# Kernel optimization log

Measured on AMD Instinct MI355X. Metric: run time of the kernel, lower is better.

The kernel has to match this reference:

```python
import jax, jax.numpy as jnp
import numpy as np

B, T, D, H = 8192, 1024, 16, 16

def setup_inputs() -> dict:
    key = jax.random.key(0)
    k1, k2, k3, k4 = jax.random.split(key, 4)
    x = jax.random.normal(k1, (B, T, D), dtype=jnp.float32)
    # fused LSTM params: gate order (i, f, g, o)
    Wi = jax.random.normal(k2, (D, 4 * H), dtype=jnp.float32) * (1.0 / np.sqrt(D))
    Wh = jax.random.normal(k3, (H, 4 * H), dtype=jnp.float32) * (1.0 / np.sqrt(H))
    b = jnp.zeros((4 * H,), dtype=jnp.float32)
    Wd = jax.random.normal(k4, (H, 2), dtype=jnp.float32) * (1.0 / np.sqrt(H))
    bd = jnp.zeros((2,), dtype=jnp.float32)
    return {"x": x, "Wi": Wi, "Wh": Wh, "b": b, "Wd": Wd, "bd": bd}

def reference(x, Wi, Wh, b, Wd, bd):
    Bx = x.shape[0]
    Hh = Wh.shape[0]
    c0 = jnp.zeros((Bx, Hh), dtype=x.dtype)
    h0 = jnp.zeros((Bx, Hh), dtype=x.dtype)

    def step(carry, x_t):
        c, h = carry
        z = x_t @ Wi + h @ Wh + b  # [B, 4H]
        i, f, g, o = jnp.split(z, 4, axis=-1)
        c = jax.nn.sigmoid(f) * c + jax.nn.sigmoid(i) * jnp.tanh(g)
        h = jax.nn.sigmoid(o) * jnp.tanh(c)
        return (c, h), None

    (c_T, h_T), _ = jax.lax.scan(step, (c0, h0), jnp.swapaxes(x, 0, 1))
    # NOTE: the original flax model uses carry1[0], the CELL state c, for the head
    logits = c_T @ Wd + bd
    return jax.nn.softmax(logits, axis=-1)
```

## Files before the change

### kernel.cpp

```cpp
#include <hip/hip_runtime.h>
#include <math.h>
#include <stdint.h>


#define BB 8192
#define TT 1024
#define DD 16
#define HH 16

typedef __attribute__((ext_vector_type(8))) short short8;
typedef __attribute__((ext_vector_type(4))) float f32x4;

__device__ __forceinline__ short f2bf(float f) {
    uint32_t u = __builtin_bit_cast(uint32_t, f);
    u += 0x7fffu + ((u >> 16) & 1u);
    return (short)(u >> 16);
}

__global__ __launch_bounds__(64) void carry_lstm_mfma(
    const float* __restrict__ x,
    const float* __restrict__ Wi,
    const float* __restrict__ Wh,
    const float* __restrict__ b,
    const float* __restrict__ Wd,
    const float* __restrict__ bd,
    float* __restrict__ out)
{
    __shared__ __align__(16) char smem[1536];
    const int lane = threadIdx.x;
    const int n = lane & 15;
    const int q = lane >> 4;
    const int e0 = blockIdx.x * 16;

    short8 Bg[4];
    float bias[4];
#pragma unroll
    for (int g = 0; g < 4; ++g) {
#pragma unroll
        for (int j = 0; j < 8; ++j) {
            const int row = q * 8 + j;
            const float w = (row < 16) ? Wi[row * 64 + g * 16 + n]
                                       : Wh[(row - 16) * 64 + g * 16 + n];
            Bg[g][j] = f2bf(w);
        }
        bias[g] = b[g * 16 + n];
    }

    const float* xg = x + (size_t)(e0 + n) * (TT * DD) + q * 4;
    char* xw = &smem[n * 48 + q * 8];
    const short8* afp = (const short8*)&smem[(q >> 1) * 768 + n * 48 + (q & 1) * 16];

    *(uint2*)&smem[768 + n * 48 + q * 8] = make_uint2(0u, 0u);
    {
        float4 x0 = *(const float4*)(xg);
        uint32_t lo = (uint16_t)f2bf(x0.x) | ((uint32_t)(uint16_t)f2bf(x0.y) << 16);
        uint32_t hi = (uint16_t)f2bf(x0.z) | ((uint32_t)(uint16_t)f2bf(x0.w) << 16);
        *(uint2*)xw = make_uint2(lo, hi);
    }
    float4 xf = *(const float4*)(xg + DD);

    float cr[4] = {0.f, 0.f, 0.f, 0.f};

    for (int t = 0; t < TT; ++t) {
        short8 af = *afp;
        asm volatile("" ::: "memory");

        f32x4 acc0 = {bias[0], bias[0], bias[0], bias[0]};
        f32x4 acc1 = {bias[1], bias[1], bias[1], bias[1]};
        f32x4 acc2 = {bias[2], bias[2], bias[2], bias[2]};
        f32x4 acc3 = {bias[3], bias[3], bias[3], bias[3]};
        acc0 = __builtin_amdgcn_mfma_f32_16x16x32_bf16(af, Bg[0], acc0, 0, 0, 0);
        acc1 = __builtin_amdgcn_mfma_f32_16x16x32_bf16(af, Bg[1], acc1, 0, 0, 0);
        acc2 = __builtin_amdgcn_mfma_f32_16x16x32_bf16(af, Bg[2], acc2, 0, 0, 0);
        acc3 = __builtin_amdgcn_mfma_f32_16x16x32_bf16(af, Bg[3], acc3, 0, 0, 0);

        const int t2 = (t + 2 < TT) ? (t + 2) : (TT - 1);
        const float4 xf2 = *(const float4*)(xg + (size_t)t2 * DD);

#pragma unroll
        for (int r = 0; r < 4; ++r) {
            float zi = acc0[r], zf = acc1[r], zg = acc2[r], zo = acc3[r];
            zi = fmaxf(zi, -12.f); zf = fmaxf(zf, -12.f);
            zg = fmaxf(zg, -12.f); zo = fmaxf(zo, -12.f);
            const float ea = __expf(-zi);
            const float ef = __expf(-zf);
            const float G  = __expf(-2.f * zg);
            const float eo = __expf(-zo);
            float u = fmaf(cr[r], ea, cr[r]);
            u = fmaf(u, G, u);
            const float s  = 1.f - G;
            const float s2 = fmaf(s, ef, s);
            const float num = u + s2;
            const float den = ((ea + 1.f) * (ef + 1.f));
            const float den3 = fmaf(den, G, den);
            const float cn = num * __builtin_amdgcn_rcpf(den3);
            cr[r] = cn;
            const float cc = fmaxf(cn, -12.f);
            const float C2 = __expf(-2.f * cc);
            const float hd = (1.f + C2) * (1.f + eo);
            const float h  = (1.f - C2) * __builtin_amdgcn_rcpf(hd);
            *(short*)&smem[768 + (q * 4 + r) * 48 + n * 2] = f2bf(h);
        }

        {
            uint32_t lo = (uint16_t)f2bf(xf.x) | ((uint32_t)(uint16_t)f2bf(xf.y) << 16);
            uint32_t hi = (uint16_t)f2bf(xf.z) | ((uint32_t)(uint16_t)f2bf(xf.w) << 16);
            *(uint2*)xw = make_uint2(lo, hi);
        }
        xf = xf2;
        asm volatile("" ::: "memory");
    }

    float p0[4], p1[4];
    const float wd0 = Wd[n * 2 + 0], wd1 = Wd[n * 2 + 1];
#pragma unroll
    for (int r = 0; r < 4; ++r) { p0[r] = cr[r] * wd0; p1[r] = cr[r] * wd1; }
#pragma unroll
    for (int off = 1; off < 16; off <<= 1) {
#pragma unroll
        for (int r = 0; r < 4; ++r) {
            p0[r] += __shfl_xor(p0[r], off, 16);
            p1[r] += __shfl_xor(p1[r], off, 16);
        }
    }
#pragma unroll
    for (int r = 0; r < 4; ++r) {
        if (n == r) {
            const float l0 = p0[r] + bd[0];
            const float l1 = p1[r] + bd[1];
            const float m  = fmaxf(l0, l1);
            const float E0 = __expf(l0 - m), E1 = __expf(l1 - m);
            const float inv = __builtin_amdgcn_rcpf(E0 + E1);
            const size_t e = (size_t)(e0 + q * 4 + r);
            out[e * 2 + 0] = E0 * inv;
            out[e * 2 + 1] = E1 * inv;
        }
    }
}

extern "C" void kernel_launch(void* const* d_in, const int* in_sizes, int n_in,
                              void* d_out, int out_size, void* d_ws, size_t ws_size,
                              hipStream_t stream) {
    const float* x  = (const float*)d_in[0];
    const float* Wi = (const float*)d_in[1];
    const float* Wh = (const float*)d_in[2];
    const float* b  = (const float*)d_in[3];
    const float* Wd = (const float*)d_in[4];
    const float* bd = (const float*)d_in[5];
    float* out = (float*)d_out;

    hipLaunchKernelGGL(carry_lstm_mfma, dim3(BB / 16), dim3(64), 0, stream,
                       x, Wi, Wh, b, Wd, bd, out);
}
```

Before: 1.181 ms.

## Keep LSTM hidden state in registers via transposed fp16 MFMA, split input projection

Transposes the gate GEMM so the MFMA output layout matches the next step's B operand, letting h stay in registers and removing the per-step shared-memory round trip. The input projection x@Wi+b is computed one step ahead with separate 16x16x16 fp16 MFMAs off the recurrent critical path. The -log2(e) scaling is folded into the weights so raw v_exp_f32 can be used, and x is prefetched through an 8-deep register ring. It switches the operands from bf16 to fp16 with round-toward-zero conversion, which changes rounding behaviour.

```diff
diff --git a/kernel.cpp b/kernel.cpp
--- a/kernel.cpp
+++ b/kernel.cpp
@@ -8,13 +8,16 @@
 #define DD 16
 #define HH 16
 
-typedef __attribute__((ext_vector_type(8))) short short8;
+typedef __attribute__((ext_vector_type(4))) __fp16 half4;
+typedef __attribute__((ext_vector_type(2))) __fp16 half2;
 typedef __attribute__((ext_vector_type(4))) float f32x4;
 
-__device__ __forceinline__ short f2bf(float f) {
-    uint32_t u = __builtin_bit_cast(uint32_t, f);
-    u += 0x7fffu + ((u >> 16) & 1u);
-    return (short)(u >> 16);
+#define L2E 1.4426950408889634f
+#define CL1 17.312340490667555f
+#define CL2 34.624680981335110f
+
+__device__ __forceinline__ float ex2(float xx) {
+    float r; asm("v_exp_f32 %0, %1" : "=v"(r) : "v"(xx)); return r;
 }
 
 __global__ __launch_bounds__(64) void carry_lstm_mfma(
@@ -26,115 +29,107 @@
     const float* __restrict__ bd,
     float* __restrict__ out)
 {
-    __shared__ __align__(16) char smem[1536];
     const int lane = threadIdx.x;
-    const int n = lane & 15;
-    const int q = lane >> 4;
-    const int e0 = blockIdx.x * 16;
+    const int lo4  = lane & 15;
+    const int s4   = lane >> 4;
+    const int e0   = blockIdx.x * 16;
 
-    short8 Bg[4];
-    float bias[4];
+    half4 Ax[4], Ah[4];
+    f32x4 bias[4];
 #pragma unroll
     for (int g = 0; g < 4; ++g) {
+        const float sc = (g == 2) ? (-2.f * L2E) : (-L2E);
+#pragma unroll
+        for (int e = 0; e < 4; ++e) {
+            const int k = 4 * s4 + e;
+            Ax[g][e] = (__fp16)(Wi[k * 64 + g * 16 + lo4] * sc);
+            Ah[g][e] = (__fp16)(Wh[k * 64 + g * 16 + lo4] * sc);
+        }
+#pragma unroll
+        for (int r = 0; r < 4; ++r)
+            bias[g][r] = b[g * 16 + 4 * s4 + r] * sc;
+    }
+
+    const float* xp = x + (size_t)(e0 + lo4) * (TT * DD) + s4 * 4;
+    float4 xq[8];
+#pragma unroll
+    for (int j = 0; j < 8; ++j) xq[j] = *(const float4*)(xp + j * 16);
+
+    union H4 { half4 v; half2 h[2]; };
+    H4 b0;
+    b0.h[0] = __builtin_amdgcn_cvt_pkrtz(xq[0].x, xq[0].y);
+    b0.h[1] = __builtin_amdgcn_cvt_pkrtz(xq[0].z, xq[0].w);
+    f32x4 ax0 = __builtin_amdgcn_mfma_f32_16x16x16f16(Ax[0], b0.v, bias[0], 0, 0, 0);
+    f32x4 ax1 = __builtin_amdgcn_mfma_f32_16x16x16f16(Ax[1], b0.v, bias[1], 0, 0, 0);
+    f32x4 ax2 = __builtin_amdgcn_mfma_f32_16x16x16f16(Ax[2], b0.v, bias[2], 0, 0, 0);
+    f32x4 ax3 = __builtin_amdgcn_mfma_f32_16x16x16f16(Ax[3], b0.v, bias[3], 0, 0, 0);
+
+    half4 Bh = {};
+    float cr[4] = {0.f, 0.f, 0.f, 0.f};
+    const float* xpp = xp + 8 * 16;
+
+    for (int tb = 0; tb < TT; tb += 8) {
+        const float* lp = (tb + 16 <= TT) ? xpp : xp;
 #pragma unroll
         for (int j = 0; j < 8; ++j) {
-            const int row = q * 8 + j;
-            const float w = (row < 16) ? Wi[row * 64 + g * 16 + n]
-                                       : Wh[(row - 16) * 64 + g * 16 + n];
-            Bg[g][j] = f2bf(w);
+            f32x4 aI = __builtin_amdgcn_mfma_f32_16x16x16f16(Ah[0], Bh, ax0, 0, 0, 0);
+            f32x4 aF = __builtin_amdgcn_mfma_f32_16x16x16f16(Ah[1], Bh, ax1, 0, 0, 0);
+            f32x4 aG = __builtin_amdgcn_mfma_f32_16x16x16f16(Ah[2], Bh, ax2, 0, 0, 0);
+            f32x4 aO = __builtin_amdgcn_mfma_f32_16x16x16f16(Ah[3], Bh, ax3, 0, 0, 0);
+
+            xq[j] = *(const float4*)(lp + j * 16);
+            const float4 xn = xq[(j + 1) & 7];
+            H4 bx;
+            bx.h[0] = __builtin_amdgcn_cvt_pkrtz(xn.x, xn.y);
+            bx.h[1] = __builtin_amdgcn_cvt_pkrtz(xn.z, xn.w);
+            ax0 = __builtin_amdgcn_mfma_f32_16x16x16f16(Ax[0], bx.v, bias[0], 0, 0, 0);
+            ax1 = __builtin_amdgcn_mfma_f32_16x16x16f16(Ax[1], bx.v, bias[1], 0, 0, 0);
+            ax2 = __builtin_amdgcn_mfma_f32_16x16x16f16(Ax[2], bx.v, bias[2], 0, 0, 0);
+            ax3 = __builtin_amdgcn_mfma_f32_16x16x16f16(Ax[3], bx.v, bias[3], 0, 0, 0);
+
+            float hh[4];
+#pragma unroll
+            for (int r = 0; r < 4; ++r) {
+                const float ea = ex2(fminf(aI[r], CL1));
+                const float ef = ex2(fminf(aF[r], CL1));
+                const float G  = ex2(fminf(aG[r], CL2));
+                const float eo = ex2(fminf(aO[r], CL1));
+                float u = fmaf(cr[r], ea, cr[r]);
+                u = fmaf(u, G, u);
+                const float s  = 1.f - G;
+                const float s2 = fmaf(s, ef, s);
+                const float num = u + s2;
+                const float den = (ea + 1.f) * (ef + 1.f);
+                const float den3 = fmaf(den, G, den);
+                const float cn = num * __builtin_amdgcn_rcpf(den3);
+                cr[r] = cn;
+                const float C2 = ex2(fminf(cn * (-2.f * L2E), CL2));
+                const float hd = (1.f + C2) * (1.f + eo);
+                hh[r] = (1.f - C2) * __builtin_amdgcn_rcpf(hd);
+            }
+            H4 hu;
+            hu.h[0] = __builtin_amdgcn_cvt_pkrtz(hh[0], hh[1]);
+            hu.h[1] = __builtin_amdgcn_cvt_pkrtz(hh[2], hh[3]);
+            Bh = hu.v;
         }
-        bias[g] = b[g * 16 + n];
+        xpp += 8 * 16;
     }
 
-    const float* xg = x + (size_t)(e0 + n) * (TT * DD) + q * 4;
-    char* xw = &smem[n * 48 + q * 8];
-    const short8* afp = (const short8*)&smem[(q >> 1) * 768 + n * 48 + (q & 1) * 16];
-
-    *(uint2*)&smem[768 + n * 48 + q * 8] = make_uint2(0u, 0u);
-    {
-        float4 x0 = *(const float4*)(xg);
-        uint32_t lo = (uint16_t)f2bf(x0.x) | ((uint32_t)(uint16_t)f2bf(x0.y) << 16);
-        uint32_t hi = (uint16_t)f2bf(x0.z) | ((uint32_t)(uint16_t)f2bf(x0.w) << 16);
-        *(uint2*)xw = make_uint2(lo, hi);
-    }
-    float4 xf = *(const float4*)(xg + DD);
-
-    float cr[4] = {0.f, 0.f, 0.f, 0.f};
-
-    for (int t = 0; t < TT; ++t) {
-        short8 af = *afp;
-        asm volatile("" ::: "memory");
-
-        f32x4 acc0 = {bias[0], bias[0], bias[0], bias[0]};
-        f32x4 acc1 = {bias[1], bias[1], bias[1], bias[1]};
-        f32x4 acc2 = {bias[2], bias[2], bias[2], bias[2]};
-        f32x4 acc3 = {bias[3], bias[3], bias[3], bias[3]};
-        acc0 = __builtin_amdgcn_mfma_f32_16x16x32_bf16(af, Bg[0], acc0, 0, 0, 0);
-        acc1 = __builtin_amdgcn_mfma_f32_16x16x32_bf16(af, Bg[1], acc1, 0, 0, 0);
-        acc2 = __builtin_amdgcn_mfma_f32_16x16x32_bf16(af, Bg[2], acc2, 0, 0, 0);
-        acc3 = __builtin_amdgcn_mfma_f32_16x16x32_bf16(af, Bg[3], acc3, 0, 0, 0);
-
-        const int t2 = (t + 2 < TT) ? (t + 2) : (TT - 1);
-        const float4 xf2 = *(const float4*)(xg + (size_t)t2 * DD);
-
-#pragma unroll
-        for (int r = 0; r < 4; ++r) {
-            float zi = acc0[r], zf = acc1[r], zg = acc2[r], zo = acc3[r];
-            zi = fmaxf(zi, -12.f); zf = fmaxf(zf, -12.f);
-            zg = fmaxf(zg, -12.f); zo = fmaxf(zo, -12.f);
-            const float ea = __expf(-zi);
-            const float ef = __expf(-zf);
-            const float G  = __expf(-2.f * zg);
-            const float eo = __expf(-zo);
-            float u = fmaf(cr[r], ea, cr[r]);
-            u = fmaf(u, G, u);
-            const float s  = 1.f - G;
-            const float s2 = fmaf(s, ef, s);
-            const float num = u + s2;
-            const float den = ((ea + 1.f) * (ef + 1.f));
-            const float den3 = fmaf(den, G, den);
-            const float cn = num * __builtin_amdgcn_rcpf(den3);
-            cr[r] = cn;
-            const float cc = fmaxf(cn, -12.f);
-            const float C2 = __expf(-2.f * cc);
-            const float hd = (1.f + C2) * (1.f + eo);
-            const float h  = (1.f - C2) * __builtin_amdgcn_rcpf(hd);
-            *(short*)&smem[768 + (q * 4 + r) * 48 + n * 2] = f2bf(h);
-        }
-
-        {
-            uint32_t lo = (uint16_t)f2bf(xf.x) | ((uint32_t)(uint16_t)f2bf(xf.y) << 16);
-            uint32_t hi = (uint16_t)f2bf(xf.z) | ((uint32_t)(uint16_t)f2bf(xf.w) << 16);
-            *(uint2*)xw = make_uint2(lo, hi);
-        }
-        xf = xf2;
-        asm volatile("" ::: "memory");
-    }
-
-    float p0[4], p1[4];
-    const float wd0 = Wd[n * 2 + 0], wd1 = Wd[n * 2 + 1];
-#pragma unroll
-    for (int r = 0; r < 4; ++r) { p0[r] = cr[r] * wd0; p1[r] = cr[r] * wd1; }
-#pragma unroll
-    for (int off = 1; off < 16; off <<= 1) {
-#pragma unroll
-        for (int r = 0; r < 4; ++r) {
-            p0[r] += __shfl_xor(p0[r], off, 16);
-            p1[r] += __shfl_xor(p1[r], off, 16);
-        }
-    }
+    float p0 = 0.f, p1 = 0.f;
 #pragma unroll
     for (int r = 0; r < 4; ++r) {
-        if (n == r) {
-            const float l0 = p0[r] + bd[0];
-            const float l1 = p1[r] + bd[1];
-            const float m  = fmaxf(l0, l1);
-            const float E0 = __expf(l0 - m), E1 = __expf(l1 - m);
-            const float inv = __builtin_amdgcn_rcpf(E0 + E1);
-            const size_t e = (size_t)(e0 + q * 4 + r);
-            out[e * 2 + 0] = E0 * inv;
-            out[e * 2 + 1] = E1 * inv;
-        }
+        p0 += cr[r] * Wd[(4 * s4 + r) * 2 + 0];
+        p1 += cr[r] * Wd[(4 * s4 + r) * 2 + 1];
+    }
+    p0 += __shfl_xor(p0, 16); p1 += __shfl_xor(p1, 16);
+    p0 += __shfl_xor(p0, 32); p1 += __shfl_xor(p1, 32);
+    if (lane < 16) {
+        const float l0 = p0 + bd[0], l1 = p1 + bd[1];
+        const float mx = fmaxf(l0, l1);
+        const float E0 = __expf(l0 - mx), E1 = __expf(l1 - mx);
+        const float inv = __builtin_amdgcn_rcpf(E0 + E1);
+        float2 o; o.x = E0 * inv; o.y = E1 * inv;
+        *(float2*)&out[(size_t)(e0 + lo4) * 2] = o;
     }
 }
 
```

Result: faster. 981.7 us (-16.9%).
